# Optimization experiments

Hardware: AMD Instinct MI355X
Metric: run time of the kernel (lower is better)

## Reference

```python
import jax, jax.numpy as jnp
import numpy as np

Q_MAX = 127.0          # 2**(8-1) - 1
QUANTILE = 0.99
GAMMA_MIN, GAMMA_MAX = 0.1, 10.0


def setup_inputs() -> dict:
    key = jax.random.key(0)
    k1, _ = jax.random.split(key)
    x = jax.random.normal(k1, (4, 4096, 2048), dtype=jnp.float32)
    gamma = jnp.ones((1,), dtype=jnp.float32)
    return {"x": x, "gamma": gamma}


def reference(x, gamma):
    # --- quantile of |x| (torch: x.flatten().abs().sort().values[k]) ---
    n = x.size
    k = int(round(QUANTILE * n))
    x_abs = jnp.abs(x.ravel())
    # faithful to full-sort-then-index (the kernel-headroom target)
    q_quantile = jax.lax.stop_gradient(jnp.sort(x_abs)[k])

    # first call: buffer initialized to q_quantile, then EMA with itself
    # -> effective running quantile == q_quantile on this step.
    gamma_c = jnp.clip(gamma, GAMMA_MIN, GAMMA_MAX)  # in-place data clamp in torch
    scale = (q_quantile / Q_MAX) * gamma_c            # shape (1,)

    # omniquant: affine fake-quantize with straight-through estimator
    xq = jnp.clip(jnp.round(x / scale), -Q_MAX - 1.0, Q_MAX) * scale
    out = x + jax.lax.stop_gradient(xq - x)           # STE
    return out
```

## Files before the change

kernel.cpp:

```cpp
#include <hip/hip_runtime.h>
#include <math.h>

typedef unsigned int u32;
typedef float nfloat4 __attribute__((ext_vector_type(4)));


#define G1 0
#define CS 2048
#define BC 3072
#define FLAG 3076
#define H2S 4096
#define H2W (4096 + (1 << 20))
#define ZERO_SLOW (4096 + (1 << 20))
#define ZERO_FAST (4096 + (1 << 20) + 3 * (1 << 20))
#define WIN_LO 1025u
#define WIN_HI 1027u
#define LOBITS (WIN_LO << 20)
#define SPANBITS ((WIN_HI - WIN_LO + 1u) << 20)

__global__ __launch_bounds__(1024) void scan_top(const u32* __restrict__ x,
                                                 u32* __restrict__ ws,
                                                 long long n, int do_cap) {
  u32* bc = ws + BC;
  u32* h2w = ws + H2W;
  __shared__ u32 red[16][4];
  const int t = threadIdx.x;

  u32 bel = 0, w0 = 0, w2 = 0, tk = 0;

  const long long n4 = n >> 2;
  const uint4* x4 = (const uint4*)x;

#define PROC(raw)                                          \
  do {                                                     \
    const u32 a_ = (raw) & 0x7fffffffu;                    \
    const u32 d_ = a_ - LOBITS;                            \
    const bool in_ = d_ < SPANBITS;                        \
    bel += (a_ < LOBITS) ? 1u : 0u;                        \
    tk += in_ ? 1u : 0u;                                   \
    w0 += (in_ && d_ < (1u << 20)) ? 1u : 0u;              \
    w2 += (in_ && d_ >= (2u << 20)) ? 1u : 0u;             \
    if (do_cap && in_) atomicAdd(&h2w[d_], 1u);            \
  } while (0)
#define PROC4(v) do { PROC((v).x); PROC((v).y); PROC((v).z); PROC((v).w); } while (0)

  const long long CH = (long long)gridDim.x * 4096;
  long long i = (long long)blockIdx.x * 4096 + t;
  for (; i + 3072 < n4; i += CH) {
    uint4 va = x4[i];
    uint4 vb = x4[i + 1024];
    uint4 vc = x4[i + 2048];
    uint4 vd = x4[i + 3072];
    PROC4(va);
    PROC4(vb);
    PROC4(vc);
    PROC4(vd);
  }
  for (int q = 0; q < 3; ++q, i += 1024)
    if (i < n4) {
      uint4 v = x4[i];
      PROC4(v);
    }
  for (long long j = (n4 << 2) + (long long)blockIdx.x * 1024 + t; j < n;
       j += (long long)gridDim.x * 1024)
    PROC(x[j]);
#undef PROC4
#undef PROC

#pragma unroll
  for (int off = 32; off > 0; off >>= 1) {
    bel += __shfl_down(bel, off, 64);
    w0 += __shfl_down(w0, off, 64);
    w2 += __shfl_down(w2, off, 64);
    tk += __shfl_down(tk, off, 64);
  }
  if ((t & 63) == 0) {
    const int w = t >> 6;
    red[w][0] = bel;
    red[w][1] = w0;
    red[w][2] = w2;
    red[w][3] = tk;
  }
  __syncthreads();
  if (t == 0) {
    u32 B = 0, W0 = 0, W2 = 0, TK = 0;
#pragma unroll
    for (int w = 0; w < 16; ++w) {
      B += red[w][0];
      W0 += red[w][1];
      W2 += red[w][2];
      TK += red[w][3];
    }
    if (B) atomicAdd(&bc[0], B);
    if (W0) atomicAdd(&bc[1], W0);
    const u32 W1 = TK - W0 - W2;
    if (W1) atomicAdd(&bc[2], W1);
    if (W2) atomicAdd(&bc[3], W2);
  }
}

__global__ __launch_bounds__(1024) void fb_top(const u32* __restrict__ x,
                                               u32* __restrict__ ws,
                                               long long n, u32 k, int force) {
  __shared__ u32 h[2048 * 8];
  __shared__ int bad;
  const int t = threadIdx.x;
  if (t == 0) {
    bad = force;
    if (!force) {
      const u32 below = ws[BC], W0 = ws[BC + 1], W1 = ws[BC + 2],
                W2 = ws[BC + 3];
      if (k < below || (k - below) >= W0 + W1 + W2) bad = 1;
    }
  }
  __syncthreads();
  if (!bad) return;
  if (t == 0) ws[FLAG] = 1u;

  u32* g1 = ws + G1;
  for (int i = t; i < 2048 * 8; i += 1024) h[i] = 0;
  __syncthreads();
  const u32 r = (u32)(t & 7);
  const long long n4 = n >> 2;
  const long long stride = (long long)gridDim.x * 1024;
  const uint4* x4 = (const uint4*)x;
  for (long long i = (long long)blockIdx.x * 1024 + t; i < n4; i += stride) {
    uint4 v = x4[i];
    atomicAdd(&h[(((v.x & 0x7fffffffu) >> 20) << 3) + r], 1u);
    atomicAdd(&h[(((v.y & 0x7fffffffu) >> 20) << 3) + r], 1u);
    atomicAdd(&h[(((v.z & 0x7fffffffu) >> 20) << 3) + r], 1u);
    atomicAdd(&h[(((v.w & 0x7fffffffu) >> 20) << 3) + r], 1u);
  }
  for (long long i = (n4 << 2) + (long long)blockIdx.x * 1024 + t; i < n;
       i += stride)
    atomicAdd(&h[(((x[i] & 0x7fffffffu) >> 20) << 3) + r], 1u);
  __syncthreads();
  for (int i = t; i < 2048; i += 1024) {
    u32 c = 0;
#pragma unroll
    for (int j = 0; j < 8; ++j) c += h[(i << 3) + j];
    if (c) atomicAdd(&g1[i], c);
  }
}

__global__ __launch_bounds__(1024) void fb_low(const u32* __restrict__ x,
                                               u32* __restrict__ ws,
                                               long long n, u32 k) {
  __shared__ u32 s[1024];
  __shared__ u32 resB1;
  if (ws[FLAG] == 0u) return;

  const u32* g1 = ws + G1;
  u32* h2 = ws + H2S;
  const int t = threadIdx.x;
  {
    const uint2 c2 = ((const uint2*)g1)[t];
    const u32 sum = c2.x + c2.y;
    s[t] = sum;
    __syncthreads();
    for (int off = 1; off < 1024; off <<= 1) {
      u32 add = (t >= off) ? s[t - off] : 0u;
      __syncthreads();
      s[t] += add;
      __syncthreads();
    }
    u32 ex = s[t] - sum;
    if (k >= ex && k < ex + c2.x) resB1 = 2 * t;
    ex += c2.x;
    if (k >= ex && k < ex + c2.y) resB1 = 2 * t + 1;
    __syncthreads();
  }
  const u32 B1 = resB1;

  const long long n4 = n >> 2;
  const long long stride = (long long)gridDim.x * 1024;
  const uint4* x4 = (const uint4*)x;
  for (long long i = (long long)blockIdx.x * 1024 + t; i < n4; i += stride) {
    uint4 v = x4[i];
    u32 a;
    a = v.x & 0x7fffffffu; if ((a >> 20) == B1) atomicAdd(&h2[a & 0xFFFFFu], 1u);
    a = v.y & 0x7fffffffu; if ((a >> 20) == B1) atomicAdd(&h2[a & 0xFFFFFu], 1u);
    a = v.z & 0x7fffffffu; if ((a >> 20) == B1) atomicAdd(&h2[a & 0xFFFFFu], 1u);
    a = v.w & 0x7fffffffu; if ((a >> 20) == B1) atomicAdd(&h2[a & 0xFFFFFu], 1u);
  }
  for (long long i = (n4 << 2) + (long long)blockIdx.x * 1024 + t; i < n;
       i += stride) {
    const u32 a = x[i] & 0x7fffffffu;
    if ((a >> 20) == B1) atomicAdd(&h2[a & 0xFFFFFu], 1u);
  }
}

__global__ __launch_bounds__(256) void chunk_reduce(u32* __restrict__ ws,
                                                    u32 k) {
  const int t = threadIdx.x;
  const u32* base;
  if (ws[FLAG] != 0u) {
    base = ws + H2S;
  } else {
    const u32 below = ws[BC], W0 = ws[BC + 1], W1 = ws[BC + 2];
    const u32 sub = k - below;
    const u32 slot = (sub < W0) ? 0u : ((sub < W0 + W1) ? 1u : 2u);
    base = ws + H2W + ((size_t)slot << 20);
  }
  u32* cs = ws + CS;
  uint4 v = ((const uint4*)(base + (size_t)blockIdx.x * 1024))[t];
  u32 sum = v.x + v.y + v.z + v.w;
#pragma unroll
  for (int off = 32; off > 0; off >>= 1) sum += __shfl_down(sum, off, 64);
  __shared__ u32 w[4];
  if ((t & 63) == 0) w[t >> 6] = sum;
  __syncthreads();
  if (t == 0) cs[blockIdx.x] = w[0] + w[1] + w[2] + w[3];
}

__global__ __launch_bounds__(1024) void quantize(const float* __restrict__ x,
                                                 float* __restrict__ out,
                                                 const u32* __restrict__ ws,
                                                 const float* __restrict__ gamma,
                                                 long long n, u32 k) {
  __shared__ u32 s[1024];
  __shared__ u32 r0, r1;
  __shared__ float fscale;
  const u32* cs = ws + CS;
  const int t = threadIdx.x;
  const int flag = (ws[FLAG] != 0u);

  u32 B1, k1;
  const u32* h2base;
  if (!flag) {
    const u32 below = ws[BC], W0 = ws[BC + 1], W1 = ws[BC + 2];
    const u32 sub = k - below;
    u32 slot;
    if (sub < W0) {
      slot = 0u; k1 = sub;
    } else if (sub < W0 + W1) {
      slot = 1u; k1 = sub - W0;
    } else {
      slot = 2u; k1 = sub - W0 - W1;
    }
    B1 = WIN_LO + slot;
    h2base = ws + H2W + ((size_t)slot << 20);
  } else {
    const uint2 c2 = ((const uint2*)(ws + G1))[t];
    const u32 sum = c2.x + c2.y;
    s[t] = sum;
    __syncthreads();
    for (int off = 1; off < 1024; off <<= 1) {
      u32 add = (t >= off) ? s[t - off] : 0u;
      __syncthreads();
      s[t] += add;
      __syncthreads();
    }
    u32 ex = s[t] - sum;
    if (k >= ex && k < ex + c2.x) { r0 = 2u * t; r1 = k - ex; }
    ex += c2.x;
    if (k >= ex && k < ex + c2.y) { r0 = 2u * t + 1u; r1 = k - ex; }
    __syncthreads();
    B1 = r0; k1 = r1;
    h2base = ws + H2S;
  }
  u32 chunk, k2;
  {
    const u32 c = cs[t];
    __syncthreads();
    s[t] = c;
    __syncthreads();
    for (int off = 1; off < 1024; off <<= 1) {
      u32 add = (t >= off) ? s[t - off] : 0u;
      __syncthreads();
      s[t] += add;
      __syncthreads();
    }
    u32 ex = s[t] - c;
    if (k1 >= ex && k1 < ex + c) { r0 = (u32)t; r1 = k1 - ex; }
    __syncthreads();
    chunk = r0; k2 = r1;
  }
  {
    const u32 c = h2base[(size_t)chunk * 1024 + t];
    __syncthreads();
    s[t] = c;
    __syncthreads();
    for (int off = 1; off < 1024; off <<= 1) {
      u32 add = (t >= off) ? s[t - off] : 0u;
      __syncthreads();
      s[t] += add;
      __syncthreads();
    }
    u32 ex = s[t] - c;
    if (k2 >= ex && k2 < ex + c) {
      const u32 bits = (B1 << 20) | (chunk * 1024u + (u32)t);
      const float q = __uint_as_float(bits);
      float gm = gamma[0];
      gm = fminf(fmaxf(gm, 0.1f), 10.0f);
      fscale = (q / 127.0f) * gm;
    }
    __syncthreads();
  }
  const float scale = fscale;

  const long long n4 = n >> 2;
  const float4* x4 = (const float4*)x;
  nfloat4* o4 = (nfloat4*)out;
#define QUANT(v, o)                                              \
  do {                                                           \
    (o).x = fminf(fmaxf(rintf((v).x / scale), -128.0f), 127.0f) * scale; \
    (o).y = fminf(fmaxf(rintf((v).y / scale), -128.0f), 127.0f) * scale; \
    (o).z = fminf(fmaxf(rintf((v).z / scale), -128.0f), 127.0f) * scale; \
    (o).w = fminf(fmaxf(rintf((v).w / scale), -128.0f), 127.0f) * scale; \
  } while (0)

  const long long CH = (long long)gridDim.x * 2048;
  long long i = (long long)blockIdx.x * 2048 + t;
  for (; i + 1024 < n4; i += CH) {
    float4 va = x4[i];
    float4 vb = x4[i + 1024];
    nfloat4 oa, ob;
    QUANT(va, oa);
    QUANT(vb, ob);
    __builtin_nontemporal_store(oa, &o4[i]);
    __builtin_nontemporal_store(ob, &o4[i + 1024]);
  }
  if (i < n4) {
    float4 v = x4[i];
    nfloat4 o;
    QUANT(v, o);
    __builtin_nontemporal_store(o, &o4[i]);
  }
#undef QUANT
  for (long long j = (n4 << 2) + (long long)blockIdx.x * 1024 + t; j < n;
       j += (long long)gridDim.x * 1024) {
    float v = x[j];
    out[j] = fminf(fmaxf(rintf(v / scale), -128.0f), 127.0f) * scale;
  }
}

extern "C" void kernel_launch(void* const* d_in, const int* in_sizes, int n_in,
                              void* d_out, int out_size, void* d_ws,
                              size_t ws_size, hipStream_t stream) {
  const u32* xbits = (const u32*)d_in[0];
  const float* gamma = (const float*)d_in[1];
  const long long n = (long long)in_sizes[0];
  u32* ws = (u32*)d_ws;

  const u32 k = (u32)llround(0.99 * (double)n);
  const int cap_ok = (ws_size >= (size_t)ZERO_FAST * sizeof(u32)) ? 1 : 0;
  const size_t zero_u32 = cap_ok ? (size_t)ZERO_FAST : (size_t)ZERO_SLOW;

  (void)hipMemsetAsync(ws, 0, zero_u32 * sizeof(u32), stream);
  scan_top<<<512, 1024, 0, stream>>>(xbits, ws, n, cap_ok);
  fb_top<<<512, 1024, 0, stream>>>(xbits, ws, n, k, cap_ok ? 0 : 1);
  fb_low<<<512, 1024, 0, stream>>>(xbits, ws, n, k);
  chunk_reduce<<<1024, 256, 0, stream>>>(ws, k);
  quantize<<<512, 1024, 0, stream>>>((const float*)d_in[0], (float*)d_out, ws,
                                     gamma, n, k);
}
```

Baseline: 274.0 us.

## Fuse quantile-select and quantize pipeline into one cooperative persistent kernel

Replaces the memset plus five separate kernel launches with a single cooperative-groups kernel that zeroes the workspace, scans, builds histograms, reduces chunks, selects the quantile and quantizes, with grid.sync() between phases. The goal is to remove launch gaps and inter-kernel drain overhead. It falls back to the old multi-kernel path if cooperative launch is unavailable or the workspace is too small. Grid-wide barriers and a grid capped by occupancy (at most 512 blocks of 1024 threads with a 64KB shared histogram) may reduce parallelism and add synchronisation cost.

Result: slower. 368.7 us (+34.6%).

```diff
diff --git a/kernel.cpp b/kernel.cpp
--- a/kernel.cpp
+++ b/kernel.cpp
@@ -1,5 +1,8 @@
 #include <hip/hip_runtime.h>
+#include <hip/hip_cooperative_groups.h>
 #include <math.h>
+
+namespace cg = cooperative_groups;
 
 typedef unsigned int u32;
 typedef float nfloat4 __attribute__((ext_vector_type(4)));
@@ -18,6 +21,304 @@
 #define LOBITS (WIN_LO << 20)
 #define SPANBITS ((WIN_HI - WIN_LO + 1u) << 20)
 
+#define PROC_BODY(raw)                                     \
+  do {                                                     \
+    const u32 a_ = (raw) & 0x7fffffffu;                    \
+    const u32 d_ = a_ - LOBITS;                            \
+    const bool in_ = d_ < SPANBITS;                        \
+    bel += (a_ < LOBITS) ? 1u : 0u;                        \
+    tk += in_ ? 1u : 0u;                                   \
+    w0 += (in_ && d_ < (1u << 20)) ? 1u : 0u;              \
+    w2 += (in_ && d_ >= (2u << 20)) ? 1u : 0u;             \
+    if (in_) atomicAdd(&h2w[d_], 1u);                      \
+  } while (0)
+
+__global__ __launch_bounds__(1024, 8) void fused_all(
+    const u32* __restrict__ x, float* __restrict__ out, u32* __restrict__ ws,
+    const float* __restrict__ gamma, long long n, u32 k) {
+  cg::grid_group grid = cg::this_grid();
+  __shared__ u32 h[2048 * 8];
+  __shared__ u32 red[16][4];
+  __shared__ u32 r0, r1;
+  __shared__ float fscale;
+  const int t = threadIdx.x;
+  const long long NB = gridDim.x;
+  const long long GT = NB * 1024;
+  const long long n4 = n >> 2;
+
+  for (long long i = (long long)blockIdx.x * 1024 + t; i < (long long)ZERO_FAST;
+       i += GT)
+    ws[i] = 0u;
+  grid.sync();
+
+  {
+    u32* bc = ws + BC;
+    u32* h2w = ws + H2W;
+    u32 bel = 0, w0 = 0, w2 = 0, tk = 0;
+    const uint4* x4 = (const uint4*)x;
+#define PROC4(v)                                                           \
+  do { PROC_BODY((v).x); PROC_BODY((v).y); PROC_BODY((v).z); PROC_BODY((v).w); } while (0)
+    const long long CH = NB * 4096;
+    long long i = (long long)blockIdx.x * 4096 + t;
+    for (; i + 3072 < n4; i += CH) {
+      uint4 va = x4[i];
+      uint4 vb = x4[i + 1024];
+      uint4 vc = x4[i + 2048];
+      uint4 vd = x4[i + 3072];
+      PROC4(va);
+      PROC4(vb);
+      PROC4(vc);
+      PROC4(vd);
+    }
+    for (int q = 0; q < 3; ++q, i += 1024)
+      if (i < n4) {
+        uint4 v = x4[i];
+        PROC4(v);
+      }
+    for (long long j = (n4 << 2) + (long long)blockIdx.x * 1024 + t; j < n;
+         j += GT)
+      PROC_BODY(x[j]);
+#undef PROC4
+#pragma unroll
+    for (int off = 32; off > 0; off >>= 1) {
+      bel += __shfl_down(bel, off, 64);
+      w0 += __shfl_down(w0, off, 64);
+      w2 += __shfl_down(w2, off, 64);
+      tk += __shfl_down(tk, off, 64);
+    }
+    if ((t & 63) == 0) {
+      const int w = t >> 6;
+      red[w][0] = bel;
+      red[w][1] = w0;
+      red[w][2] = w2;
+      red[w][3] = tk;
+    }
+    __syncthreads();
+    if (t == 0) {
+      u32 B = 0, W0 = 0, W2 = 0, TK = 0;
+#pragma unroll
+      for (int w = 0; w < 16; ++w) {
+        B += red[w][0];
+        W0 += red[w][1];
+        W2 += red[w][2];
+        TK += red[w][3];
+      }
+      if (B) atomicAdd(&bc[0], B);
+      if (W0) atomicAdd(&bc[1], W0);
+      const u32 W1 = TK - W0 - W2;
+      if (W1) atomicAdd(&bc[2], W1);
+      if (W2) atomicAdd(&bc[3], W2);
+    }
+  }
+  grid.sync();
+
+  const u32 below = ws[BC], W0 = ws[BC + 1], W1 = ws[BC + 2], W2 = ws[BC + 3];
+  const bool bad = (k < below) || ((k - below) >= W0 + W1 + W2);
+
+  if (bad) {
+    {
+      u32* g1 = ws + G1;
+      for (int i = t; i < 2048 * 8; i += 1024) h[i] = 0;
+      __syncthreads();
+      const u32 r = (u32)(t & 7);
+      const uint4* x4 = (const uint4*)x;
+      for (long long i = (long long)blockIdx.x * 1024 + t; i < n4; i += GT) {
+        uint4 v = x4[i];
+        atomicAdd(&h[(((v.x & 0x7fffffffu) >> 20) << 3) + r], 1u);
+        atomicAdd(&h[(((v.y & 0x7fffffffu) >> 20) << 3) + r], 1u);
+        atomicAdd(&h[(((v.z & 0x7fffffffu) >> 20) << 3) + r], 1u);
+        atomicAdd(&h[(((v.w & 0x7fffffffu) >> 20) << 3) + r], 1u);
+      }
+      for (long long i = (n4 << 2) + (long long)blockIdx.x * 1024 + t; i < n;
+           i += GT)
+        atomicAdd(&h[(((x[i] & 0x7fffffffu) >> 20) << 3) + r], 1u);
+      __syncthreads();
+      for (int i = t; i < 2048; i += 1024) {
+        u32 c = 0;
+#pragma unroll
+        for (int j = 0; j < 8; ++j) c += h[(i << 3) + j];
+        if (c) atomicAdd(&g1[i], c);
+      }
+    }
+    grid.sync();
+    {
+      u32* s = h;
+      const u32* g1 = ws + G1;
+      u32* h2 = ws + H2S;
+      const uint2 c2 = ((const uint2*)g1)[t];
+      const u32 sum = c2.x + c2.y;
+      s[t] = sum;
+      __syncthreads();
+      for (int off = 1; off < 1024; off <<= 1) {
+        u32 add = (t >= off) ? s[t - off] : 0u;
+        __syncthreads();
+        s[t] += add;
+        __syncthreads();
+      }
+      u32 ex = s[t] - sum;
+      if (k >= ex && k < ex + c2.x) r0 = 2u * t;
+      ex += c2.x;
+      if (k >= ex && k < ex + c2.y) r0 = 2u * t + 1u;
+      __syncthreads();
+      const u32 B1 = r0;
+      const uint4* x4 = (const uint4*)x;
+      for (long long i = (long long)blockIdx.x * 1024 + t; i < n4; i += GT) {
+        uint4 v = x4[i];
+        u32 a;
+        a = v.x & 0x7fffffffu; if ((a >> 20) == B1) atomicAdd(&h2[a & 0xFFFFFu], 1u);
+        a = v.y & 0x7fffffffu; if ((a >> 20) == B1) atomicAdd(&h2[a & 0xFFFFFu], 1u);
+        a = v.z & 0x7fffffffu; if ((a >> 20) == B1) atomicAdd(&h2[a & 0xFFFFFu], 1u);
+        a = v.w & 0x7fffffffu; if ((a >> 20) == B1) atomicAdd(&h2[a & 0xFFFFFu], 1u);
+      }
+      for (long long i = (n4 << 2) + (long long)blockIdx.x * 1024 + t; i < n;
+           i += GT) {
+        const u32 a = x[i] & 0x7fffffffu;
+        if ((a >> 20) == B1) atomicAdd(&h2[a & 0xFFFFFu], 1u);
+      }
+      __syncthreads();
+    }
+    grid.sync();
+  }
+
+  {
+    const u32* base;
+    u32 slot = 0;
+    if (bad) {
+      base = ws + H2S;
+    } else {
+      const u32 sub = k - below;
+      slot = (sub < W0) ? 0u : ((sub < W0 + W1) ? 1u : 2u);
+      base = ws + H2W + ((size_t)slot << 20);
+    }
+    u32* cs = ws + CS;
+    for (u32 c = (u32)blockIdx.x; c < 1024u; c += (u32)NB) {
+      u32 sum = base[(size_t)c * 1024 + t];
+#pragma unroll
+      for (int off = 32; off > 0; off >>= 1) sum += __shfl_down(sum, off, 64);
+      if ((t & 63) == 0) red[t >> 6][0] = sum;
+      __syncthreads();
+      if (t == 0) {
+        u32 s16 = 0;
+#pragma unroll
+        for (int w = 0; w < 16; ++w) s16 += red[w][0];
+        cs[c] = s16;
+      }
+      __syncthreads();
+    }
+  }
+  grid.sync();
+
+  {
+    u32* s = h;
+    const u32* cs = ws + CS;
+    u32 B1, k1;
+    const u32* h2base;
+    if (!bad) {
+      const u32 sub = k - below;
+      u32 slot;
+      if (sub < W0) {
+        slot = 0u; k1 = sub;
+      } else if (sub < W0 + W1) {
+        slot = 1u; k1 = sub - W0;
+      } else {
+        slot = 2u; k1 = sub - W0 - W1;
+      }
+      B1 = WIN_LO + slot;
+      h2base = ws + H2W + ((size_t)slot << 20);
+    } else {
+      const uint2 c2 = ((const uint2*)(ws + G1))[t];
+      const u32 sum = c2.x + c2.y;
+      s[t] = sum;
+      __syncthreads();
+      for (int off = 1; off < 1024; off <<= 1) {
+        u32 add = (t >= off) ? s[t - off] : 0u;
+        __syncthreads();
+        s[t] += add;
+        __syncthreads();
+      }
+      u32 ex = s[t] - sum;
+      if (k >= ex && k < ex + c2.x) { r0 = 2u * t; r1 = k - ex; }
+      ex += c2.x;
+      if (k >= ex && k < ex + c2.y) { r0 = 2u * t + 1u; r1 = k - ex; }
+      __syncthreads();
+      B1 = r0; k1 = r1;
+      h2base = ws + H2S;
+    }
+    u32 chunk, k2;
+    {
+      const u32 c = cs[t];
+      __syncthreads();
+      s[t] = c;
+      __syncthreads();
+      for (int off = 1; off < 1024; off <<= 1) {
+        u32 add = (t >= off) ? s[t - off] : 0u;
+        __syncthreads();
+        s[t] += add;
+        __syncthreads();
+      }
+      u32 ex = s[t] - c;
+      if (k1 >= ex && k1 < ex + c) { r0 = (u32)t; r1 = k1 - ex; }
+      __syncthreads();
+      chunk = r0; k2 = r1;
+    }
+    {
+      const u32 c = h2base[(size_t)chunk * 1024 + t];
+      __syncthreads();
+      s[t] = c;
+      __syncthreads();
+      for (int off = 1; off < 1024; off <<= 1) {
+        u32 add = (t >= off) ? s[t - off] : 0u;
+        __syncthreads();
+        s[t] += add;
+        __syncthreads();
+      }
+      u32 ex = s[t] - c;
+      if (k2 >= ex && k2 < ex + c) {
+        const u32 bits = (B1 << 20) | (chunk * 1024u + (u32)t);
+        const float q = __uint_as_float(bits);
+        float gm = gamma[0];
+        gm = fminf(fmaxf(gm, 0.1f), 10.0f);
+        fscale = (q / 127.0f) * gm;
+      }
+      __syncthreads();
+    }
+    const float scale = fscale;
+
+    const float4* x4 = (const float4*)x;
+    nfloat4* o4 = (nfloat4*)out;
+#define QUANT(v, o)                                                        \
+  do {                                                                     \
+    (o).x = fminf(fmaxf(rintf((v).x / scale), -128.0f), 127.0f) * scale;   \
+    (o).y = fminf(fmaxf(rintf((v).y / scale), -128.0f), 127.0f) * scale;   \
+    (o).z = fminf(fmaxf(rintf((v).z / scale), -128.0f), 127.0f) * scale;   \
+    (o).w = fminf(fmaxf(rintf((v).w / scale), -128.0f), 127.0f) * scale;   \
+  } while (0)
+    const long long CH = NB * 2048;
+    long long i = (long long)blockIdx.x * 2048 + t;
+    for (; i + 1024 < n4; i += CH) {
+      float4 va = x4[i];
+      float4 vb = x4[i + 1024];
+      nfloat4 oa, ob;
+      QUANT(va, oa);
+      QUANT(vb, ob);
+      __builtin_nontemporal_store(oa, &o4[i]);
+      __builtin_nontemporal_store(ob, &o4[i + 1024]);
+    }
+    if (i < n4) {
+      float4 v = x4[i];
+      nfloat4 o;
+      QUANT(v, o);
+      __builtin_nontemporal_store(o, &o4[i]);
+    }
+#undef QUANT
+    for (long long j = (n4 << 2) + (long long)blockIdx.x * 1024 + t; j < n;
+         j += GT) {
+      float v = x[j];
+      out[j] = fminf(fmaxf(rintf(v / scale), -128.0f), 127.0f) * scale;
+    }
+  }
+}
+
 __global__ __launch_bounds__(1024) void scan_top(const u32* __restrict__ x,
                                                  u32* __restrict__ ws,
                                                  long long n, int do_cap) {
@@ -25,12 +326,9 @@
   u32* h2w = ws + H2W;
   __shared__ u32 red[16][4];
   const int t = threadIdx.x;
-
   u32 bel = 0, w0 = 0, w2 = 0, tk = 0;
-
   const long long n4 = n >> 2;
   const uint4* x4 = (const uint4*)x;
-
 #define PROC(raw)                                          \
   do {                                                     \
     const u32 a_ = (raw) & 0x7fffffffu;                    \
@@ -43,7 +341,6 @@
     if (do_cap && in_) atomicAdd(&h2w[d_], 1u);            \
   } while (0)
 #define PROC4(v) do { PROC((v).x); PROC((v).y); PROC((v).z); PROC((v).w); } while (0)
-
   const long long CH = (long long)gridDim.x * 4096;
   long long i = (long long)blockIdx.x * 4096 + t;
   for (; i + 3072 < n4; i += CH) {
@@ -66,7 +363,6 @@
     PROC(x[j]);
 #undef PROC4
 #undef PROC
-
 #pragma unroll
   for (int off = 32; off > 0; off >>= 1) {
     bel += __shfl_down(bel, off, 64);
@@ -302,14 +598,13 @@
   const long long n4 = n >> 2;
   const float4* x4 = (const float4*)x;
   nfloat4* o4 = (nfloat4*)out;
-#define QUANT(v, o)                                              \
-  do {                                                           \
-    (o).x = fminf(fmaxf(rintf((v).x / scale), -128.0f), 127.0f) * scale; \
-    (o).y = fminf(fmaxf(rintf((v).y / scale), -128.0f), 127.0f) * scale; \
-    (o).z = fminf(fmaxf(rintf((v).z / scale), -128.0f), 127.0f) * scale; \
-    (o).w = fminf(fmaxf(rintf((v).w / scale), -128.0f), 127.0f) * scale; \
+#define QUANT(v, o)                                                        \
+  do {                                                                     \
+    (o).x = fminf(fmaxf(rintf((v).x / scale), -128.0f), 127.0f) * scale;   \
+    (o).y = fminf(fmaxf(rintf((v).y / scale), -128.0f), 127.0f) * scale;   \
+    (o).z = fminf(fmaxf(rintf((v).z / scale), -128.0f), 127.0f) * scale;   \
+    (o).w = fminf(fmaxf(rintf((v).w / scale), -128.0f), 127.0f) * scale;   \
   } while (0)
-
   const long long CH = (long long)gridDim.x * 2048;
   long long i = (long long)blockIdx.x * 2048 + t;
   for (; i + 1024 < n4; i += CH) {
@@ -340,18 +635,51 @@
                               size_t ws_size, hipStream_t stream) {
   const u32* xbits = (const u32*)d_in[0];
   const float* gamma = (const float*)d_in[1];
-  const long long n = (long long)in_sizes[0];
+  float* outp = (float*)d_out;
+  long long n = (long long)in_sizes[0];
   u32* ws = (u32*)d_ws;
-
-  const u32 k = (u32)llround(0.99 * (double)n);
+  u32 k = (u32)llround(0.99 * (double)n);
+
   const int cap_ok = (ws_size >= (size_t)ZERO_FAST * sizeof(u32)) ? 1 : 0;
-  const size_t zero_u32 = cap_ok ? (size_t)ZERO_FAST : (size_t)ZERO_SLOW;
-
-  (void)hipMemsetAsync(ws, 0, zero_u32 * sizeof(u32), stream);
-  scan_top<<<512, 1024, 0, stream>>>(xbits, ws, n, cap_ok);
-  fb_top<<<512, 1024, 0, stream>>>(xbits, ws, n, k, cap_ok ? 0 : 1);
-  fb_low<<<512, 1024, 0, stream>>>(xbits, ws, n, k);
-  chunk_reduce<<<1024, 256, 0, stream>>>(ws, k);
-  quantize<<<512, 1024, 0, stream>>>((const float*)d_in[0], (float*)d_out, ws,
-                                     gamma, n, k);
+
+  static int coop_grid = -2;
+  if (coop_grid == -2) {
+    int dev = 0;
+    (void)hipGetDevice(&dev);
+    int coop = 0, ncu = 0, nb = 0;
+    (void)hipDeviceGetAttribute(&coop, hipDeviceAttributeCooperativeLaunch, dev);
+    (void)hipDeviceGetAttribute(&ncu, hipDeviceAttributeMultiprocessorCount,
+                                dev);
+    hipError_t e =
+        hipOccupancyMaxActiveBlocksPerMultiprocessor(&nb, fused_all, 1024, 0);
+    if (coop && e == hipSuccess && nb >= 1 && ncu > 0) {
+      long long g = (long long)nb * ncu;
+      coop_grid = (int)((g > 512) ? 512 : g);
+    } else {
+      coop_grid = 0;
+    }
+  }
+
+  bool launched = false;
+  if (cap_ok && coop_grid >= 256) {
+    void* args[] = {(void*)&xbits, (void*)&outp, (void*)&ws,
+                    (void*)&gamma, (void*)&n,    (void*)&k};
+    hipError_t e = hipLaunchCooperativeKernel(fused_all, dim3(coop_grid),
+                                              dim3(1024), args, 0, stream);
+    if (e == hipSuccess)
+      launched = true;
+    else
+      coop_grid = 0;
+  }
+
+  if (!launched) {
+    const size_t zero_u32 = cap_ok ? (size_t)ZERO_FAST : (size_t)ZERO_SLOW;
+    (void)hipMemsetAsync(ws, 0, zero_u32 * sizeof(u32), stream);
+    scan_top<<<512, 1024, 0, stream>>>(xbits, ws, n, cap_ok);
+    fb_top<<<512, 1024, 0, stream>>>(xbits, ws, n, k, cap_ok ? 0 : 1);
+    fb_low<<<512, 1024, 0, stream>>>(xbits, ws, n, k);
+    chunk_reduce<<<1024, 256, 0, stream>>>(ws, k);
+    quantize<<<512, 1024, 0, stream>>>((const float*)d_in[0], outp, ws, gamma,
+                                       n, k);
+  }
 }
```

## Narrow fast-path capture window to a fine bit range around the quantile

Applied to the files above, without the earlier changes.

Replaces the three-exponent capture window (1M bins each) with a single fine window of 256K raw-bit bins starting at 0x40230000, which is tuned to where the 0.99 quantile of |N(0,1)| lies. Fewer elements fall inside the window, so the scan issues far fewer global atomics, fewer counters are reduced, and only 256 chunks need summing. The fallback full-histogram path still runs if k is not inside the window, but the window is tuned to the test distribution.

Measured after the change: 260.4 us. 1.05x faster.

```diff
diff --git a/kernel.cpp b/kernel.cpp
--- a/kernel.cpp
+++ b/kernel.cpp
@@ -10,37 +10,32 @@
 #define BC 3072
 #define FLAG 3076
 #define H2S 4096
-#define H2W (4096 + (1 << 20))
+#define H2F (4096 + (1 << 20))
 #define ZERO_SLOW (4096 + (1 << 20))
-#define ZERO_FAST (4096 + (1 << 20) + 3 * (1 << 20))
-#define WIN_LO 1025u
-#define WIN_HI 1027u
-#define LOBITS (WIN_LO << 20)
-#define SPANBITS ((WIN_HI - WIN_LO + 1u) << 20)
+#define ZERO_FAST (4096 + (1 << 20) + (1 << 18))
+#define FINE_LO 0x40230000u
+#define FINE_SPAN 0x40000u
 
 __global__ __launch_bounds__(1024) void scan_top(const u32* __restrict__ x,
                                                  u32* __restrict__ ws,
                                                  long long n, int do_cap) {
   u32* bc = ws + BC;
-  u32* h2w = ws + H2W;
-  __shared__ u32 red[16][4];
-  const int t = threadIdx.x;
-
-  u32 bel = 0, w0 = 0, w2 = 0, tk = 0;
-
+  u32* h2f = ws + H2F;
+  __shared__ u32 red[16][2];
+  const int t = threadIdx.x;
+  u32 clo = 0, cin = 0;
   const long long n4 = n >> 2;
   const uint4* x4 = (const uint4*)x;
 
 #define PROC(raw)                                          \
   do {                                                     \
     const u32 a_ = (raw) & 0x7fffffffu;                    \
-    const u32 d_ = a_ - LOBITS;                            \
-    const bool in_ = d_ < SPANBITS;                        \
-    bel += (a_ < LOBITS) ? 1u : 0u;                        \
-    tk += in_ ? 1u : 0u;                                   \
-    w0 += (in_ && d_ < (1u << 20)) ? 1u : 0u;              \
-    w2 += (in_ && d_ >= (2u << 20)) ? 1u : 0u;             \
-    if (do_cap && in_) atomicAdd(&h2w[d_], 1u);            \
+    const u32 d_ = a_ - FINE_LO;                           \
+    clo += (a_ < FINE_LO) ? 1u : 0u;                       \
+    if (d_ < FINE_SPAN) {                                  \
+      cin += 1u;                                           \
+      if (do_cap) atomicAdd(&h2f[d_], 1u);                 \
+    }                                                      \
   } while (0)
 #define PROC4(v) do { PROC((v).x); PROC((v).y); PROC((v).z); PROC((v).w); } while (0)
 
@@ -69,33 +64,24 @@
 
 #pragma unroll
   for (int off = 32; off > 0; off >>= 1) {
-    bel += __shfl_down(bel, off, 64);
-    w0 += __shfl_down(w0, off, 64);
-    w2 += __shfl_down(w2, off, 64);
-    tk += __shfl_down(tk, off, 64);
+    clo += __shfl_down(clo, off, 64);
+    cin += __shfl_down(cin, off, 64);
   }
   if ((t & 63) == 0) {
     const int w = t >> 6;
-    red[w][0] = bel;
-    red[w][1] = w0;
-    red[w][2] = w2;
-    red[w][3] = tk;
+    red[w][0] = clo;
+    red[w][1] = cin;
   }
   __syncthreads();
   if (t == 0) {
-    u32 B = 0, W0 = 0, W2 = 0, TK = 0;
+    u32 L = 0, I = 0;
 #pragma unroll
     for (int w = 0; w < 16; ++w) {
-      B += red[w][0];
-      W0 += red[w][1];
-      W2 += red[w][2];
-      TK += red[w][3];
-    }
-    if (B) atomicAdd(&bc[0], B);
-    if (W0) atomicAdd(&bc[1], W0);
-    const u32 W1 = TK - W0 - W2;
-    if (W1) atomicAdd(&bc[2], W1);
-    if (W2) atomicAdd(&bc[3], W2);
+      L += red[w][0];
+      I += red[w][1];
+    }
+    if (L) atomicAdd(&bc[0], L);
+    if (I) atomicAdd(&bc[1], I);
   }
 }
 
@@ -108,9 +94,8 @@
   if (t == 0) {
     bad = force;
     if (!force) {
-      const u32 below = ws[BC], W0 = ws[BC + 1], W1 = ws[BC + 2],
-                W2 = ws[BC + 3];
-      if (k < below || (k - below) >= W0 + W1 + W2) bad = 1;
+      const u32 clo = ws[BC], cin = ws[BC + 1];
+      if (k < clo || (k - clo) >= cin) bad = 1;
     }
   }
   __syncthreads();
@@ -197,10 +182,8 @@
   if (ws[FLAG] != 0u) {
     base = ws + H2S;
   } else {
-    const u32 below = ws[BC], W0 = ws[BC + 1], W1 = ws[BC + 2];
-    const u32 sub = k - below;
-    const u32 slot = (sub < W0) ? 0u : ((sub < W0 + W1) ? 1u : 2u);
-    base = ws + H2W + ((size_t)slot << 20);
+    if (blockIdx.x >= 256) return;
+    base = ws + H2F;
   }
   u32* cs = ws + CS;
   uint4 v = ((const uint4*)(base + (size_t)blockIdx.x * 1024))[t];
@@ -225,21 +208,11 @@
   const int t = threadIdx.x;
   const int flag = (ws[FLAG] != 0u);
 
-  u32 B1, k1;
+  u32 B1 = 0, k1;
   const u32* h2base;
   if (!flag) {
-    const u32 below = ws[BC], W0 = ws[BC + 1], W1 = ws[BC + 2];
-    const u32 sub = k - below;
-    u32 slot;
-    if (sub < W0) {
-      slot = 0u; k1 = sub;
-    } else if (sub < W0 + W1) {
-      slot = 1u; k1 = sub - W0;
-    } else {
-      slot = 2u; k1 = sub - W0 - W1;
-    }
-    B1 = WIN_LO + slot;
-    h2base = ws + H2W + ((size_t)slot << 20);
+    k1 = k - ws[BC];
+    h2base = ws + H2F;
   } else {
     const uint2 c2 = ((const uint2*)(ws + G1))[t];
     const u32 sum = c2.x + c2.y;
@@ -261,7 +234,7 @@
   }
   u32 chunk, k2;
   {
-    const u32 c = cs[t];
+    const u32 c = (!flag && t >= 256) ? 0u : cs[t];
     __syncthreads();
     s[t] = c;
     __syncthreads();
@@ -272,7 +245,7 @@
       __syncthreads();
     }
     u32 ex = s[t] - c;
-    if (k1 >= ex && k1 < ex + c) { r0 = (u32)t; r1 = k1 - ex; }
+    if (c && k1 >= ex && k1 < ex + c) { r0 = (u32)t; r1 = k1 - ex; }
     __syncthreads();
     chunk = r0; k2 = r1;
   }
@@ -288,8 +261,9 @@
       __syncthreads();
     }
     u32 ex = s[t] - c;
-    if (k2 >= ex && k2 < ex + c) {
-      const u32 bits = (B1 << 20) | (chunk * 1024u + (u32)t);
+    if (c && k2 >= ex && k2 < ex + c) {
+      const u32 bits = flag ? ((B1 << 20) | (chunk * 1024u + (u32)t))
+                            : (FINE_LO + chunk * 1024u + (u32)t);
       const float q = __uint_as_float(bits);
       float gm = gamma[0];
       gm = fminf(fmaxf(gm, 0.1f), 10.0f);
@@ -302,14 +276,13 @@
   const long long n4 = n >> 2;
   const float4* x4 = (const float4*)x;
   nfloat4* o4 = (nfloat4*)out;
-#define QUANT(v, o)                                              \
-  do {                                                           \
-    (o).x = fminf(fmaxf(rintf((v).x / scale), -128.0f), 127.0f) * scale; \
-    (o).y = fminf(fmaxf(rintf((v).y / scale), -128.0f), 127.0f) * scale; \
-    (o).z = fminf(fmaxf(rintf((v).z / scale), -128.0f), 127.0f) * scale; \
-    (o).w = fminf(fmaxf(rintf((v).w / scale), -128.0f), 127.0f) * scale; \
+#define QUANT(v, o)                                                        \
+  do {                                                                     \
+    (o).x = fminf(fmaxf(rintf((v).x / scale), -128.0f), 127.0f) * scale;   \
+    (o).y = fminf(fmaxf(rintf((v).y / scale), -128.0f), 127.0f) * scale;   \
+    (o).z = fminf(fmaxf(rintf((v).z / scale), -128.0f), 127.0f) * scale;   \
+    (o).w = fminf(fmaxf(rintf((v).w / scale), -128.0f), 127.0f) * scale;   \
   } while (0)
-
   const long long CH = (long long)gridDim.x * 2048;
   long long i = (long long)blockIdx.x * 2048 + t;
   for (; i + 1024 < n4; i += CH) {
```
